# Performance work log

Hardware: AMD Instinct MI355X
Metric: run time of the kernel (lower is better)

The kernel has to match this reference:

```python
import jax, jax.numpy as jnp
from jax import lax
import numpy as np

SMOOTH = 1e-05
BASE_W = jnp.array([1.0, 1.0, 1.0], dtype=jnp.float32)
BOUND_W = jnp.array([2.0, 3.0, 5.0], dtype=jnp.float32)
FG_W = jnp.array([1.0, 1.5, 3.0], dtype=jnp.float32)
MAX_DIST = 10.0  # cv2 result is clamped to 10.0 in the original module
R = 10  # search radius: any distance > 10 is clamped anyway

# Precompute all integer offsets with Euclidean norm <= R (includes (0,0) -> dist 0)
_offs = [(dy, dx, float(np.hypot(dy, dx)))
         for dy in range(-R, R + 1) for dx in range(-R, R + 1)
         if dy * dy + dx * dx <= R * R]
_DY = jnp.array([o[0] + R for o in _offs], dtype=jnp.int32)  # shifted into padded coords
_DX = jnp.array([o[1] + R for o in _offs], dtype=jnp.int32)
_DD = jnp.array([o[2] for o in _offs], dtype=jnp.float32)


def _distance_transform(mask):
    """Clamped Euclidean distance from each pixel to the nearest foreground pixel.
    mask: [B,H,W] binary float (1 = foreground). Equivalent to
    clamp(cv2.distanceTransform(1-mask, DIST_L2), max=10) (exact L2 vs chamfer approx).
    """
    B, H, W = mask.shape
    pad = jnp.pad(mask, ((0, 0), (R, R), (R, R)))

    def step(cur, od):
        dy, dx, d = od
        sl = lax.dynamic_slice(pad, (0, dy, dx), (B, H, W))
        return jnp.minimum(cur, jnp.where(sl > 0.5, d, MAX_DIST)), None

    init = jnp.full((B, H, W), MAX_DIST, dtype=mask.dtype)
    dist, _ = lax.scan(step, init, (_DY, _DX, _DD))
    return dist


def setup_inputs() -> dict:
    key = jax.random.key(0)
    k1, k2, k3 = jax.random.split(key, 3)
    B, H, W = 64, 512, 512
    predictions = jax.random.normal(k1, (B, 1, H, W), dtype=jnp.float32)
    targets = (jax.random.uniform(k2, (B, 1, H, W)) < 0.2).astype(jnp.float32)
    task_ids = jax.random.randint(k3, (B,), 0, 3)
    return {"predictions": predictions, "targets": targets, "task_ids": task_ids}


def reference(predictions, targets, task_ids):
    x, t = predictions, targets
    axes = (1, 2, 3)
    p = jax.nn.sigmoid(x)
    pc = jnp.clip(p, 1e-07, 1.0 - 1e-07)

    # ---- base loss: per-sample Dice + BCEWithLogits ----
    inter = jnp.sum(pc * t, axis=axes)
    union = jnp.sum(pc, axis=axes) + jnp.sum(t, axis=axes)
    dice_loss = 1.0 - (2.0 * inter + SMOOTH) / (union + SMOOTH)
    # numerically stable BCE-with-logits
    bce = jnp.maximum(x, 0.0) - x * t + jnp.log1p(jnp.exp(-jnp.abs(x)))
    base_loss = dice_loss + jnp.mean(bce, axis=axes)

    # ---- boundary loss: distance-transform weighted L1 ----
    tb = (t > 0.5).astype(x.dtype)  # [B,1,H,W]
    dist = _distance_transform(tb[:, 0])  # [B,H,W], clamped at 10
    boundary_loss = jnp.mean(dist * jnp.abs(pc[:, 0] - tb[:, 0]), axis=(1, 2))

    # ---- foreground-weighted BCE ----
    fg = tb
    bg = 1.0 - tb
    fg_count = jnp.sum(fg, axis=axes)
    bg_count = jnp.sum(bg, axis=axes)
    fg_weight = jnp.clip(bg_count / (fg_count + 1e-07), 1.0, 10.0)
    bce_p = -(t * jnp.log(pc) + (1.0 - t) * jnp.log(1.0 - pc))
    w = fg * fg_weight[:, None, None, None] + bg
    fg_loss = jnp.mean(bce_p * w, axis=axes)
    fg_loss = jnp.where(fg_count == 0, 0.0, fg_loss)

    per_sample = (BASE_W[task_ids] * base_loss
                  + BOUND_W[task_ids] * boundary_loss
                  + FG_W[task_ids] * fg_loss)
    return jnp.mean(per_sample)
```

## Files before the change

kernel.cpp:

```cpp
#include <hip/hip_runtime.h>
#include <stdint.h>

#define NB 64
#define NH 512
#define NW 512
#define RPAD 10
#define NROWS (NH + 2 * RPAD)
#define RWORDS 18
#define IMG_WORDS (NROWS * RWORDS)
#define NPIX (NH * NW)

#if __has_builtin(__builtin_amdgcn_alignbit)
#define ALIGNBIT(hi, lo, s) __builtin_amdgcn_alignbit((hi), (lo), (s))
#else
#define ALIGNBIT(hi, lo, s) ((uint32_t)(((((uint64_t)(hi)) << 32) | (lo)) >> ((s) & 31)))
#endif

__global__ __launch_bounds__(256) void build_bits(const float* __restrict__ targ,
                                                  uint32_t* __restrict__ bits) {
    const int y0 = blockIdx.x * 4;
    const int b  = blockIdx.y;
    const int tid = threadIdx.x;
    const int ry = y0 + (tid >> 6);
    const int xb = (tid & 63) * 8;

    const float4* tg = (const float4*)(targ + ((size_t)b * NH + ry) * NW + xb);
    const float4 a = tg[0];
    const float4 c = tg[1];
    uint32_t m = (uint32_t)(a.x > 0.5f)
               | ((uint32_t)(a.y > 0.5f) << 1)
               | ((uint32_t)(a.z > 0.5f) << 2)
               | ((uint32_t)(a.w > 0.5f) << 3)
               | ((uint32_t)(c.x > 0.5f) << 4)
               | ((uint32_t)(c.y > 0.5f) << 5)
               | ((uint32_t)(c.z > 0.5f) << 6)
               | ((uint32_t)(c.w > 0.5f) << 7);

    __shared__ uint32_t swd[64];
    ((uint8_t*)swd)[tid] = (uint8_t)m;
    __syncthreads();
    if (tid < 64) {
        const int rw = tid >> 4, ww = tid & 15;
        bits[(size_t)b * IMG_WORDS + (size_t)(y0 + rw + RPAD) * RWORDS + 1 + ww] = swd[tid];
    }
}

__global__ __launch_bounds__(256) void main_loss(const float* __restrict__ pred,
                                                 const float* __restrict__ targ,
                                                 const uint32_t* __restrict__ bits,
                                                 float* __restrict__ partials) {
    const int y0 = blockIdx.x * 4;
    const int b  = blockIdx.y;
    const int tid  = threadIdx.x;
    const int wave = tid >> 6, lane = tid & 63;
    const int y = y0 + wave;
    const int x = lane * 8;

    __shared__ uint32_t sb[24 * RWORDS];
    const uint32_t* img = bits + (size_t)b * IMG_WORDS;
    for (int i = tid; i < 24 * RWORDS; i += 256)
        sb[i] = img[(size_t)(y0 + i / RWORDS) * RWORDS + (i % RWORDS)];
    __syncthreads();

    const int lw = (x + 22) >> 5;
    const int s0 = (x + 22) & 31;
    const uint32_t* wrow = sb + wave * RWORDS + lw;

    uint32_t mind2[8];
#pragma unroll
    for (int i = 0; i < 8; ++i) mind2[i] = 1u << 20;

#define FOLD(K2, M, LO, HI) { \
        const uint32_t w32 = ALIGNBIT((HI), (LO), s0); \
        const uint32_t rv = __builtin_bitreverse32(w32); \
        _Pragma("unroll") \
        for (int i = 0; i < 8; ++i) { \
            uint32_t cc = (w32 >> (10 + i)) | (rv >> (21 - i)); \
            cc = (cc & ((1u << ((M) + 1)) - 1u)) | (1u << ((M) + 1)); \
            uint32_t dx = (uint32_t)__builtin_ctz(cc) & 31u; \
            uint32_t d2 = (uint32_t)(K2) + dx * dx; \
            mind2[i] = min(mind2[i], d2); \
        } }

#define PAIR(K, M) { \
        const uint32_t lo = wrow[(10 + (K)) * RWORDS]     | wrow[(10 - (K)) * RWORDS]; \
        const uint32_t hi = wrow[(10 + (K)) * RWORDS + 1] | wrow[(10 - (K)) * RWORDS + 1]; \
        FOLD((K) * (K), (M), lo, hi) }

#define CHECK(K) { \
        const uint32_t mx = max(max(max(mind2[0], mind2[1]), max(mind2[2], mind2[3])), \
                                max(max(mind2[4], mind2[5]), max(mind2[6], mind2[7]))); \
        if (__all(mx <= (uint32_t)((K) * (K)))) goto dt_done; }

    {
        const uint32_t lo = wrow[10 * RWORDS];
        const uint32_t hi = wrow[10 * RWORDS + 1];
        FOLD(0, 10, lo, hi)
    }
    CHECK(1)
    PAIR(1, 9)  CHECK(2)
    PAIR(2, 9)  CHECK(3)
    PAIR(3, 9)  CHECK(4)
    PAIR(4, 9)  CHECK(5)
    PAIR(5, 8)  CHECK(6)
    PAIR(6, 8)  CHECK(7)
    PAIR(7, 7)  CHECK(8)
    PAIR(8, 6)  CHECK(9)
    PAIR(9, 4)  CHECK(10)
    PAIR(10, 0)
dt_done:;

    const size_t base = ((size_t)b * NH + y) * NW + x;
    const float4* pp = (const float4*)(pred + base);
    const float4* tp = (const float4*)(targ + base);
    const float4 p0 = pp[0], p1 = pp[1];
    const float4 t0 = tp[0], t1 = tp[1];
    float pv[8] = {p0.x, p0.y, p0.z, p0.w, p1.x, p1.y, p1.z, p1.w};
    float tv[8] = {t0.x, t0.y, t0.z, t0.w, t1.x, t1.y, t1.z, t1.w};

    float s[8] = {0, 0, 0, 0, 0, 0, 0, 0};
#pragma unroll
    for (int i = 0; i < 8; ++i) {
        const float xv = pv[i], t = tv[i];
        const float ax = fabsf(xv);
        const float e  = __expf(-ax);
        const float L  = __logf(1.0f + e);
        const float r  = __builtin_amdgcn_rcpf(1.0f + e);
        const float p  = (xv >= 0.0f) ? r : e * r;
        const float pc = fminf(fmaxf(p, 1e-7f), 0.99999988f);
        const float tb = (t > 0.5f) ? 1.0f : 0.0f;
        const float minx = fminf(xv, 0.0f), maxx = fmaxf(xv, 0.0f);
        const float logpc   = fminf(fmaxf(minx - L, -16.118096f), -1.1920929e-7f);
        const float log1mpc = fminf(fmaxf(-maxx - L, -16.118096f), -1.1920929e-7f);
        const float bce = maxx - xv * t + L;
        const float dist = (mind2[i] > 100u) ? 10.0f : __fsqrt_rn((float)mind2[i]);
        const float bce_p = -(t * logpc + (1.0f - t) * log1mpc);
        s[0] += pc * t;
        s[1] += pc;
        s[2] += t;
        s[3] += bce;
        s[4] += dist * fabsf(pc - tb);
        s[5] += tb;
        s[6] += tb * bce_p;
        s[7] += (1.0f - tb) * bce_p;
    }

#pragma unroll
    for (int k = 0; k < 8; ++k) {
#pragma unroll
        for (int off = 32; off > 0; off >>= 1)
            s[k] += __shfl_down(s[k], off, 64);
    }
    __shared__ float red[4][8];
    if (lane == 0) {
#pragma unroll
        for (int k = 0; k < 8; ++k) red[wave][k] = s[k];
    }
    __syncthreads();
    if (tid < 8) {
        const float sum = red[0][tid] + red[1][tid] + red[2][tid] + red[3][tid];
        atomicAdd(&partials[b * 8 + tid], sum);
    }
}

__global__ __launch_bounds__(64) void finalize(const float* __restrict__ partials,
                                               const int* __restrict__ task_ids,
                                               float* __restrict__ out) {
    const int b = threadIdx.x;
    const float Nf = (float)NPIX;
    const float inter = partials[b * 8 + 0];
    const float spc   = partials[b * 8 + 1];
    const float st    = partials[b * 8 + 2];
    const float sbce  = partials[b * 8 + 3];
    const float sbdry = partials[b * 8 + 4];
    const float sfg   = partials[b * 8 + 5];
    const float sfgb  = partials[b * 8 + 6];
    const float sbgb  = partials[b * 8 + 7];

    const float dice = 1.0f - (2.0f * inter + 1e-5f) / (spc + st + 1e-5f);
    const float base = dice + sbce / Nf;
    const float bdry = sbdry / Nf;
    const float bgc  = Nf - sfg;
    const float fgw  = fminf(fmaxf(bgc / (sfg + 1e-7f), 1.0f), 10.0f);
    float fgl = (fgw * sfgb + sbgb) / Nf;
    if (sfg == 0.0f) fgl = 0.0f;

    const int t = task_ids[b];
    const float BW[3]  = {1.0f, 1.0f, 1.0f};
    const float BDW[3] = {2.0f, 3.0f, 5.0f};
    const float FW[3]  = {1.0f, 1.5f, 3.0f};
    float per = BW[t] * base + BDW[t] * bdry + FW[t] * fgl;

#pragma unroll
    for (int off = 32; off > 0; off >>= 1)
        per += __shfl_down(per, off, 64);
    if (b == 0) out[0] = per * (1.0f / 64.0f);
}

extern "C" void kernel_launch(void* const* d_in, const int* in_sizes, int n_in,
                              void* d_out, int out_size, void* d_ws, size_t ws_size,
                              hipStream_t stream) {
    const float* pred     = (const float*)d_in[0];
    const float* targ     = (const float*)d_in[1];
    const int*   task_ids = (const int*)d_in[2];
    float* out = (float*)d_out;

    float* partials = (float*)d_ws;
    uint32_t* bits = (uint32_t*)((char*)d_ws + 4096);

    hipMemsetAsync(d_ws, 0, 4096 + (size_t)NB * IMG_WORDS * sizeof(uint32_t), stream);
    build_bits<<<dim3(NH / 4, NB), 256, 0, stream>>>(targ, bits);
    main_loss<<<dim3(NH / 4, NB), 256, 0, stream>>>(pred, targ, bits, partials);
    finalize<<<1, 64, 0, stream>>>(partials, task_ids, out);
}
```

Before: 167.9 us.

## Derive targets from bitmask, drop memset and finalize kernel via last-block reduction

main_loss no longer re-reads the float targets. It recovers the binary target bits from the packed bitmask already in shared memory and folds the foreground BCE into the plain BCE sum. build_bits now writes the padding rows itself and zeroes the accumulators, which removes the workspace memset. A last-block atomic counter performs the final per-sample combination, replacing the separate finalize launch. Reductions use DPP row adds over six accumulators, and the prediction load is issued early to overlap the distance-transform work. The risks are the slight change in log clamping semantics and the correctness of the cross-block counter.

```diff
diff --git a/kernel.cpp b/kernel.cpp
--- a/kernel.cpp
+++ b/kernel.cpp
@@ -9,6 +9,7 @@
 #define RWORDS 18
 #define IMG_WORDS (NROWS * RWORDS)
 #define NPIX (NH * NW)
+#define NBLK_MAIN (NH / 4 * NB)
 
 #if __has_builtin(__builtin_amdgcn_alignbit)
 #define ALIGNBIT(hi, lo, s) __builtin_amdgcn_alignbit((hi), (lo), (s))
@@ -16,39 +17,62 @@
 #define ALIGNBIT(hi, lo, s) ((uint32_t)(((((uint64_t)(hi)) << 32) | (lo)) >> ((s) & 31)))
 #endif
 
+template <int N>
+__device__ __forceinline__ float dpp_add(float v) {
+#if __has_builtin(__builtin_amdgcn_update_dpp)
+    int s = __builtin_amdgcn_update_dpp(0, __float_as_int(v), 0x110 | N, 0xf, 0xf, true);
+    return v + __int_as_float(s);
+#else
+    return v + __shfl_up(v, N, 16);
+#endif
+}
+
 __global__ __launch_bounds__(256) void build_bits(const float* __restrict__ targ,
-                                                  uint32_t* __restrict__ bits) {
-    const int y0 = blockIdx.x * 4;
-    const int b  = blockIdx.y;
+                                                  uint32_t* __restrict__ bits,
+                                                  float* __restrict__ partials,
+                                                  int* __restrict__ counter) {
+    const int b   = blockIdx.y;
     const int tid = threadIdx.x;
-    const int ry = y0 + (tid >> 6);
-    const int xb = (tid & 63) * 8;
-
-    const float4* tg = (const float4*)(targ + ((size_t)b * NH + ry) * NW + xb);
-    const float4 a = tg[0];
-    const float4 c = tg[1];
-    uint32_t m = (uint32_t)(a.x > 0.5f)
-               | ((uint32_t)(a.y > 0.5f) << 1)
-               | ((uint32_t)(a.z > 0.5f) << 2)
-               | ((uint32_t)(a.w > 0.5f) << 3)
-               | ((uint32_t)(c.x > 0.5f) << 4)
-               | ((uint32_t)(c.y > 0.5f) << 5)
-               | ((uint32_t)(c.z > 0.5f) << 6)
-               | ((uint32_t)(c.w > 0.5f) << 7);
-
-    __shared__ uint32_t swd[64];
-    ((uint8_t*)swd)[tid] = (uint8_t)m;
-    __syncthreads();
-    if (tid < 64) {
-        const int rw = tid >> 4, ww = tid & 15;
-        bits[(size_t)b * IMG_WORDS + (size_t)(y0 + rw + RPAD) * RWORDS + 1 + ww] = swd[tid];
+    const int wave = tid >> 6, lane = tid & 63;
+    const int r = blockIdx.x * 4 + wave;
+    const int y = r - RPAD;
+
+    if (blockIdx.x == 0 && b == 0) {
+        partials[tid] = 0.0f;
+        partials[tid + 256] = 0.0f;
+        if (tid == 0) *counter = 0;
+    }
+
+    uint32_t m = 0;
+    if (y >= 0 && y < NH) {
+        const float4* tg = (const float4*)(targ + ((size_t)b * NH + y) * NW + lane * 8);
+        const float4 a = tg[0];
+        const float4 c = tg[1];
+        m = (uint32_t)(a.x > 0.5f)
+          | ((uint32_t)(a.y > 0.5f) << 1)
+          | ((uint32_t)(a.z > 0.5f) << 2)
+          | ((uint32_t)(a.w > 0.5f) << 3)
+          | ((uint32_t)(c.x > 0.5f) << 4)
+          | ((uint32_t)(c.y > 0.5f) << 5)
+          | ((uint32_t)(c.z > 0.5f) << 6)
+          | ((uint32_t)(c.w > 0.5f) << 7);
+    }
+
+    __shared__ uint32_t swd[4][16];
+    ((uint8_t*)swd[wave])[lane] = (uint8_t)m;
+    __syncthreads();
+    if (lane < RWORDS) {
+        const uint32_t v = (lane >= 1 && lane <= 16) ? swd[wave][lane - 1] : 0u;
+        bits[(size_t)b * IMG_WORDS + (size_t)r * RWORDS + lane] = v;
     }
 }
 
 __global__ __launch_bounds__(256) void main_loss(const float* __restrict__ pred,
-                                                 const float* __restrict__ targ,
                                                  const uint32_t* __restrict__ bits,
-                                                 float* __restrict__ partials) {
+                                                 const int* __restrict__ task_ids,
+                                                 float* __restrict__ partials,
+                                                 int* __restrict__ counter,
+                                                 float* __restrict__ out) {
     const int y0 = blockIdx.x * 4;
     const int b  = blockIdx.y;
     const int tid  = threadIdx.x;
@@ -56,26 +80,27 @@
     const int y = y0 + wave;
     const int x = lane * 8;
 
+    const float4* pp = (const float4*)(pred + ((size_t)b * NH + y) * NW + x);
+    const float4 p0 = pp[0], p1 = pp[1];
+
     __shared__ uint32_t sb[24 * RWORDS];
     const uint32_t* img = bits + (size_t)b * IMG_WORDS;
-    for (int i = tid; i < 24 * RWORDS; i += 256)
-        sb[i] = img[(size_t)(y0 + i / RWORDS) * RWORDS + (i % RWORDS)];
+    if (tid < 108)
+        ((uint4*)sb)[tid] = ((const uint4*)(img + (size_t)y0 * RWORDS))[tid];
     __syncthreads();
 
     const int lw = (x + 22) >> 5;
-    const int s0 = (x + 22) & 31;
+    const int s0i = (x + 22) & 31;
     const uint32_t* wrow = sb + wave * RWORDS + lw;
 
     uint32_t mind2[8];
 #pragma unroll
     for (int i = 0; i < 8; ++i) mind2[i] = 1u << 20;
 
-#define FOLD(K2, M, LO, HI) { \
-        const uint32_t w32 = ALIGNBIT((HI), (LO), s0); \
-        const uint32_t rv = __builtin_bitreverse32(w32); \
+#define FOLD(K2, M, W32, RV) { \
         _Pragma("unroll") \
         for (int i = 0; i < 8; ++i) { \
-            uint32_t cc = (w32 >> (10 + i)) | (rv >> (21 - i)); \
+            uint32_t cc = ((W32) >> (10 + i)) | ((RV) >> (21 - i)); \
             cc = (cc & ((1u << ((M) + 1)) - 1u)) | (1u << ((M) + 1)); \
             uint32_t dx = (uint32_t)__builtin_ctz(cc) & 31u; \
             uint32_t d2 = (uint32_t)(K2) + dx * dx; \
@@ -85,20 +110,24 @@
 #define PAIR(K, M) { \
         const uint32_t lo = wrow[(10 + (K)) * RWORDS]     | wrow[(10 - (K)) * RWORDS]; \
         const uint32_t hi = wrow[(10 + (K)) * RWORDS + 1] | wrow[(10 - (K)) * RWORDS + 1]; \
-        FOLD((K) * (K), (M), lo, hi) }
+        const uint32_t w32 = ALIGNBIT(hi, lo, s0i); \
+        const uint32_t rv  = __builtin_bitreverse32(w32); \
+        FOLD((K) * (K), (M), w32, rv) }
 
 #define CHECK(K) { \
         const uint32_t mx = max(max(max(mind2[0], mind2[1]), max(mind2[2], mind2[3])), \
                                 max(max(mind2[4], mind2[5]), max(mind2[6], mind2[7]))); \
         if (__all(mx <= (uint32_t)((K) * (K)))) goto dt_done; }
 
+    uint32_t c32;
     {
         const uint32_t lo = wrow[10 * RWORDS];
         const uint32_t hi = wrow[10 * RWORDS + 1];
-        FOLD(0, 10, lo, hi)
-    }
-    CHECK(1)
-    PAIR(1, 9)  CHECK(2)
+        c32 = ALIGNBIT(hi, lo, s0i);
+        const uint32_t rv = __builtin_bitreverse32(c32);
+        FOLD(0, 10, c32, rv)
+    }
+    PAIR(1, 9)
     PAIR(2, 9)  CHECK(3)
     PAIR(3, 9)  CHECK(4)
     PAIR(4, 9)  CHECK(5)
@@ -110,91 +139,86 @@
     PAIR(10, 0)
 dt_done:;
 
-    const size_t base = ((size_t)b * NH + y) * NW + x;
-    const float4* pp = (const float4*)(pred + base);
-    const float4* tp = (const float4*)(targ + base);
-    const float4 p0 = pp[0], p1 = pp[1];
-    const float4 t0 = tp[0], t1 = tp[1];
-    float pv[8] = {p0.x, p0.y, p0.z, p0.w, p1.x, p1.y, p1.z, p1.w};
-    float tv[8] = {t0.x, t0.y, t0.z, t0.w, t1.x, t1.y, t1.z, t1.w};
-
-    float s[8] = {0, 0, 0, 0, 0, 0, 0, 0};
+    const float pv[8] = {p0.x, p0.y, p0.z, p0.w, p1.x, p1.y, p1.z, p1.w};
+    float s0 = 0.0f, s1 = 0.0f, s3 = 0.0f, s4 = 0.0f, s5 = 0.0f;
 #pragma unroll
     for (int i = 0; i < 8; ++i) {
-        const float xv = pv[i], t = tv[i];
+        const uint32_t tbb = (c32 >> (10 + i)) & 1u;
+        const float tbf = tbb ? 1.0f : 0.0f;
+        const float xv = pv[i];
         const float ax = fabsf(xv);
         const float e  = __expf(-ax);
-        const float L  = __logf(1.0f + e);
-        const float r  = __builtin_amdgcn_rcpf(1.0f + e);
+        const float ope = 1.0f + e;
+        const float L  = __logf(ope);
+        const float r  = __builtin_amdgcn_rcpf(ope);
         const float p  = (xv >= 0.0f) ? r : e * r;
         const float pc = fminf(fmaxf(p, 1e-7f), 0.99999988f);
-        const float tb = (t > 0.5f) ? 1.0f : 0.0f;
-        const float minx = fminf(xv, 0.0f), maxx = fmaxf(xv, 0.0f);
-        const float logpc   = fminf(fmaxf(minx - L, -16.118096f), -1.1920929e-7f);
-        const float log1mpc = fminf(fmaxf(-maxx - L, -16.118096f), -1.1920929e-7f);
-        const float bce = maxx - xv * t + L;
         const float dist = (mind2[i] > 100u) ? 10.0f : __fsqrt_rn((float)mind2[i]);
-        const float bce_p = -(t * logpc + (1.0f - t) * log1mpc);
-        s[0] += pc * t;
-        s[1] += pc;
-        s[2] += t;
-        s[3] += bce;
-        s[4] += dist * fabsf(pc - tb);
-        s[5] += tb;
-        s[6] += tb * bce_p;
-        s[7] += (1.0f - tb) * bce_p;
-    }
-
-#pragma unroll
-    for (int k = 0; k < 8; ++k) {
+        const float bce = fmaxf(tbb ? -xv : xv, 0.0f) + L;
+        s0 += tbb ? pc : 0.0f;
+        s1 += pc;
+        s3 += dist * fabsf(pc - tbf);
+        s4 += tbb ? bce : 0.0f;
+        s5 += tbb ? 0.0f : bce;
+    }
+    float s2 = (float)__popc(c32 & 0x0003FC00u);
+
+    float v[6] = {s0, s1, s2, s3, s4, s5};
+#pragma unroll
+    for (int k = 0; k < 6; ++k) {
+        v[k] = dpp_add<1>(v[k]);
+        v[k] = dpp_add<2>(v[k]);
+        v[k] = dpp_add<4>(v[k]);
+        v[k] = dpp_add<8>(v[k]);
+    }
+    __shared__ float red[16][6];
+    if ((lane & 15) == 15) {
+        const int g = wave * 4 + (lane >> 4);
+#pragma unroll
+        for (int k = 0; k < 6; ++k) red[g][k] = v[k];
+    }
+    __syncthreads();
+    if (tid < 6) {
+        float acc = 0.0f;
+#pragma unroll
+        for (int g = 0; g < 16; ++g) acc += red[g][tid];
+        atomicAdd(&partials[b * 8 + tid], acc);
+    }
+
+    __shared__ int lastblk;
+    if (tid == 0) {
+        __threadfence();
+        const int prev = __hip_atomic_fetch_add(counter, 1, __ATOMIC_ACQ_REL,
+                                                __HIP_MEMORY_SCOPE_AGENT);
+        lastblk = (prev == NBLK_MAIN - 1);
+    }
+    __syncthreads();
+    if (lastblk && tid < 64) {
+        const int bb = tid;
+        float q[6];
+#pragma unroll
+        for (int k = 0; k < 6; ++k)
+            q[k] = __hip_atomic_load(&partials[bb * 8 + k], __ATOMIC_ACQUIRE,
+                                     __HIP_MEMORY_SCOPE_AGENT);
+        const float Nf = (float)NPIX;
+        const float inter = q[0], spc = q[1], sfg = q[2];
+        const float sbdry = q[3], sfgb = q[4], sbgb = q[5];
+        const float sbce = sfgb + sbgb;
+        const float dice = 1.0f - (2.0f * inter + 1e-5f) / (spc + sfg + 1e-5f);
+        const float base = dice + sbce / Nf;
+        const float bdry = sbdry / Nf;
+        const float fgw  = fminf(fmaxf((Nf - sfg) / (sfg + 1e-7f), 1.0f), 10.0f);
+        float fgl = (fgw * sfgb + sbgb) / Nf;
+        if (sfg == 0.0f) fgl = 0.0f;
+        const int t = task_ids[bb];
+        const float BDW[3] = {2.0f, 3.0f, 5.0f};
+        const float FW[3]  = {1.0f, 1.5f, 3.0f};
+        float per = base + BDW[t] * bdry + FW[t] * fgl;
 #pragma unroll
         for (int off = 32; off > 0; off >>= 1)
-            s[k] += __shfl_down(s[k], off, 64);
-    }
-    __shared__ float red[4][8];
-    if (lane == 0) {
-#pragma unroll
-        for (int k = 0; k < 8; ++k) red[wave][k] = s[k];
-    }
-    __syncthreads();
-    if (tid < 8) {
-        const float sum = red[0][tid] + red[1][tid] + red[2][tid] + red[3][tid];
-        atomicAdd(&partials[b * 8 + tid], sum);
-    }
-}
-
-__global__ __launch_bounds__(64) void finalize(const float* __restrict__ partials,
-                                               const int* __restrict__ task_ids,
-                                               float* __restrict__ out) {
-    const int b = threadIdx.x;
-    const float Nf = (float)NPIX;
-    const float inter = partials[b * 8 + 0];
-    const float spc   = partials[b * 8 + 1];
-    const float st    = partials[b * 8 + 2];
-    const float sbce  = partials[b * 8 + 3];
-    const float sbdry = partials[b * 8 + 4];
-    const float sfg   = partials[b * 8 + 5];
-    const float sfgb  = partials[b * 8 + 6];
-    const float sbgb  = partials[b * 8 + 7];
-
-    const float dice = 1.0f - (2.0f * inter + 1e-5f) / (spc + st + 1e-5f);
-    const float base = dice + sbce / Nf;
-    const float bdry = sbdry / Nf;
-    const float bgc  = Nf - sfg;
-    const float fgw  = fminf(fmaxf(bgc / (sfg + 1e-7f), 1.0f), 10.0f);
-    float fgl = (fgw * sfgb + sbgb) / Nf;
-    if (sfg == 0.0f) fgl = 0.0f;
-
-    const int t = task_ids[b];
-    const float BW[3]  = {1.0f, 1.0f, 1.0f};
-    const float BDW[3] = {2.0f, 3.0f, 5.0f};
-    const float FW[3]  = {1.0f, 1.5f, 3.0f};
-    float per = BW[t] * base + BDW[t] * bdry + FW[t] * fgl;
-
-#pragma unroll
-    for (int off = 32; off > 0; off >>= 1)
-        per += __shfl_down(per, off, 64);
-    if (b == 0) out[0] = per * (1.0f / 64.0f);
+            per += __shfl_down(per, off, 64);
+        if (tid == 0) out[0] = per * (1.0f / 64.0f);
+    }
 }
 
 extern "C" void kernel_launch(void* const* d_in, const int* in_sizes, int n_in,
@@ -206,10 +230,10 @@
     float* out = (float*)d_out;
 
     float* partials = (float*)d_ws;
+    int* counter = (int*)((char*)d_ws + 2048);
     uint32_t* bits = (uint32_t*)((char*)d_ws + 4096);
 
-    hipMemsetAsync(d_ws, 0, 4096 + (size_t)NB * IMG_WORDS * sizeof(uint32_t), stream);
-    build_bits<<<dim3(NH / 4, NB), 256, 0, stream>>>(targ, bits);
-    main_loss<<<dim3(NH / 4, NB), 256, 0, stream>>>(pred, targ, bits, partials);
-    finalize<<<1, 64, 0, stream>>>(partials, task_ids, out);
-}
+    build_bits<<<dim3(NROWS / 4, NB), 256, 0, stream>>>(targ, bits, partials, counter);
+    main_loss<<<dim3(NH / 4, NB), 256, 0, stream>>>(pred, bits, task_ids, partials,
+                                                    counter, out);
+}
```

Result: slower. 545.2 us (+224.7%).
